# Optimization experiments

Measured on AMD Instinct MI355X. Metric: run time of the kernel, lower is better.

Reference implementation:

```python
import jax, jax.numpy as jnp
import numpy as np

# dims matching input_specs / init_kwargs
S_BATCH, T_BATCH, NUM, DIM, H, W = 4, 4, 8, 512, 32, 32
K = 64              # self.k, number of kmeans clusters
KMEANS_ITERS = 10   # fixed Lloyd iterations (stand-in for kmeans-to-convergence)


def _kmeans(points):
    """Euclidean Lloyd kmeans. points: [n, d] -> centers [K, d].
    Deterministic init: first K points. Empty clusters keep old center."""
    centers0 = points[:K]
    sq_p = jnp.sum(points * points, axis=1)  # [n]

    def step(centers, _):
        # squared euclidean distance [n, K]
        d2 = sq_p[:, None] + jnp.sum(centers * centers, axis=1)[None, :] \
             - 2.0 * points @ centers.T
        assign = jnp.argmin(d2, axis=1)                      # [n]
        onehot = jax.nn.one_hot(assign, K, dtype=points.dtype)  # [n, K]
        counts = onehot.sum(axis=0)                          # [K]
        sums = onehot.T @ points                             # [K, d]
        new = jnp.where(counts[:, None] > 0,
                        sums / jnp.maximum(counts, 1.0)[:, None],
                        centers)
        return new, None

    centers, _ = jax.lax.scan(step, centers0, None, length=KMEANS_ITERS)
    return centers


def setup_inputs() -> dict:
    key = jax.random.key(0)
    k1, k2, k3, k4 = jax.random.split(key, 4)
    return {
        "source_feat": jax.random.normal(k1, (S_BATCH, NUM, DIM, H, W), dtype=jnp.float32),
        "target_feat": jax.random.normal(k2, (T_BATCH, NUM, DIM, H, W), dtype=jnp.float32),
        "source_label": jax.random.randint(k3, (S_BATCH,), 0, 10),
        "target_label": jax.random.randint(k4, (T_BATCH,), 0, 10),
    }


def reference(source_feat, target_feat, source_label, target_label):
    sb, num, dim, h, w = source_feat.shape
    tb = target_feat.shape[0]

    # view each map as (h*w, dim) point cloud, kmeans per (batch, num)
    s_pts = source_feat.reshape(sb, num, dim, h * w).transpose(0, 1, 3, 2)
    t_pts = target_feat.reshape(tb, num, dim, h * w).transpose(0, 1, 3, 2)
    km = jax.vmap(jax.vmap(_kmeans))
    cs = km(s_pts).transpose(1, 0, 2, 3)  # [num, sb, K, dim]
    ct = km(t_pts).transpose(1, 0, 2, 3)  # [num, tb, K, dim]

    # mat_dist for every (num, i, j) pair of center sets: [num, sb, tb, K, K]
    sq_s = jnp.sum(cs * cs, axis=-1)  # [num, sb, K]
    sq_t = jnp.sum(ct * ct, axis=-1)  # [num, tb, K]
    dots = jnp.einsum('nikd,njld->nijkl', cs, ct)
    dist = jnp.sqrt(jnp.maximum(
        sq_s[:, :, None, :, None] + sq_t[:, None, :, None, :] - 2.0 * dots, 0.0))
    y = jnp.argmin(dist, axis=-1)  # [num, sb, tb, K] nearest target center per source center

    # gather matched target centers; replicate source centers over j (torch append order: i, j, k)
    ct_b = jnp.broadcast_to(ct[:, None], (num, sb, tb, K, dim))
    t_mat = jnp.take_along_axis(ct_b, y[..., None], axis=3)            # [num, sb, tb, K, dim]
    s_mat = jnp.broadcast_to(cs[:, :, None], (num, sb, tb, K, dim))

    N = sb * tb * K
    s_mat = s_mat.reshape(num, N, dim)
    t_mat = t_mat.reshape(num, N, dim)

    # trans_mat[k] = s_mat.T @ pinv(t_mat.T)   -> [num, dim, dim]
    pinv_t = jnp.linalg.pinv(t_mat.transpose(0, 2, 1))  # pinv([dim, N]) -> [num, N, dim]
    trans_mat = jnp.einsum('nkd,nke->nde', s_mat, pinv_t)
    return trans_mat
```

## Files before the change

kernel.cpp:

```cpp
#include <hip/hip_runtime.h>

typedef unsigned int u32;
typedef unsigned long long u64;

#define NPTS  1024
#define DIMD  512
#define KCL   64
#define KMIT  10

constexpr size_t O_CTG  = 0;
constexpr size_t O_SUMS = O_CTG  + 64ull*512*64;
constexpr size_t O_CNT  = O_SUMS + 64ull*64*512;
constexpr size_t O_SQC  = O_CNT  + 64ull*64;
constexpr size_t O_SQP  = O_SQC  + 64ull*64;
constexpr size_t O_ASG  = O_SQP  + 64ull*1024;
constexpr size_t O_CTN  = O_ASG  + 64ull*1024;
constexpr size_t O_Y    = O_CTN  + 8ull*256*512;
constexpr size_t O_CNT2 = O_Y    + 8ull*4*4*64;
constexpr size_t O_BM   = O_CNT2 + 8ull*256;
constexpr size_t O_G    = O_BM   + 8ull*256*512;
constexpr size_t O_LT   = O_G    + 8ull*256*256;
constexpr size_t O_YB   = O_LT   + 8ull*256*256;
constexpr size_t O_ZB   = O_YB   + 8ull*256*512;
constexpr size_t O_PTST = O_ZB   + 8ull*256*512;

constexpr size_t O_PS0 = O_SUMS;
constexpr size_t O_PS1 = O_CTN;
static_assert(O_PS1 + 64ull*64*512 <= O_G, "PS1 overlay must fit before O_G");

constexpr size_t O_CS = O_SUMS;
constexpr size_t O_W  = O_YB;
constexpr size_t O_WT = O_YB + 8ull*4*64*64;

__device__ __forceinline__ const float* run_base(const float* s, const float* t, int run){
    const float* b = (run < 32) ? s : t;
    return b + (size_t)(run & 31) * (DIMD * NPTS);
}
__device__ __forceinline__ u64 dpack(float d2, int c){
    u32 u = __float_as_uint(d2);
    u = (u & 0x80000000u) ? ~u : (u | 0x80000000u);
    return ((u64)u << 32) | (u32)c;
}
__device__ __forceinline__ float rdlane(float v, int l){
    return __uint_as_float(__builtin_amdgcn_readlane(__float_as_uint(v), l));
}

__global__ __launch_bounds__(256) void k_init(const float* __restrict__ src, const float* __restrict__ tgt,
                                              float* __restrict__ ws){
    int bx = blockIdx.x; int run = bx >> 2, q = bx & 3;
    int tid = threadIdx.x;
    const float* base = run_base(src, tgt, run);
    int p = q*256 + tid;
    float acc = 0.f;
    for (int d = 0; d < DIMD; ++d){
        float v = base[(size_t)d*NPTS + p];
        acc = fmaf(v, v, acc);
    }
    ws[O_SQP + run*NPTS + p] = acc;
    if (q == 0){
        if (tid < KCL) ws[O_SQC + run*KCL + tid] = acc;
        if (tid < KCL) ((int*)(ws + O_CNT))[run*KCL + tid] = 0;
        for (int idx = tid; idx < DIMD*KCL; idx += 256){
            int d = idx >> 6, c = idx & 63;
            ws[O_CTG + (size_t)run*DIMD*KCL + idx] = base[(size_t)d*NPTS + c];
        }
    }
}

__global__ __launch_bounds__(256) void k_ptsT(const float* __restrict__ src, const float* __restrict__ tgt,
                                              float* __restrict__ ws){
    int bx = blockIdx.x; int dt = bx & 7, pt = (bx >> 3) & 15, run = bx >> 7;
    int tid = threadIdx.x, lane = tid & 63, r4 = tid >> 6;
    const float* base = run_base(src, tgt, run);
    __shared__ float t[64*65];
    for (int pass = 0; pass < 16; ++pass){
        int r = pass*4 + r4;
        t[r*65 + lane] = base[(size_t)(dt*64 + r)*NPTS + pt*64 + lane];
    }
    __syncthreads();
    for (int pass = 0; pass < 16; ++pass){
        int p = pass*4 + r4;
        ws[O_PTST + ((size_t)run*NPTS + pt*64 + p)*DIMD + dt*64 + lane] = t[lane*65 + p];
    }
}

__global__ __launch_bounds__(256) void k_assign(const float* __restrict__ src, const float* __restrict__ tgt,
                                                const float* __restrict__ ctr, const float* __restrict__ sqc,
                                                const float* __restrict__ sqp,
                                                int* __restrict__ asg, int* __restrict__ cnt){
    int bx = blockIdx.x; int run = bx >> 3, qt = bx & 7;
    int tid = threadIdx.x, lane = tid & 63;
    int g = __builtin_amdgcn_readfirstlane(tid >> 6);
    const float* base = run_base(src, tgt, run);
    const float* cg = ctr + (size_t)run*DIMD*KCL + g*16;
    int p0 = qt*128 + 2*lane;
    float acc[2][16] = {};
    __shared__ u64 red[4][128];

#define LOADP(P, DB) { \
    _Pragma("unroll") \
    for (int u = 0; u < 8; ++u) \
        P[u] = *(const float2*)&base[(size_t)((DB)*8 + u)*NPTS + p0]; }

#define COMPUTE(P, DB) { \
    _Pragma("unroll") \
    for (int u = 0; u < 8; ++u){ \
        const float4* cp = (const float4*)(cg + (size_t)((DB)*8 + u)*KCL); \
        float4 c0 = cp[0], c1 = cp[1], c2 = cp[2], c3 = cp[3]; \
        float cv[16] = {c0.x,c0.y,c0.z,c0.w, c1.x,c1.y,c1.z,c1.w, \
                        c2.x,c2.y,c2.z,c2.w, c3.x,c3.y,c3.z,c3.w}; \
        _Pragma("unroll") \
        for (int cl = 0; cl < 16; ++cl){ \
            acc[0][cl] = fmaf(P[u].x, cv[cl], acc[0][cl]); \
            acc[1][cl] = fmaf(P[u].y, cv[cl], acc[1][cl]); \
        } \
    } }

    float2 pa[8], pb[8];
    LOADP(pa, 0);
    for (int db = 0; db < 64; db += 2){
        if (db + 1 < 64) LOADP(pb, db + 1);
        COMPUTE(pa, db);
        if (db + 2 < 64) LOADP(pa, db + 2);
        COMPUTE(pb, db + 1);
    }
#undef LOADP
#undef COMPUTE

    const float* sqcg = sqc + run*KCL + g*16;
    float sq[16];
    #pragma unroll
    for (int q = 0; q < 16; ++q) sq[q] = sqcg[q];
    float2 sq2 = *(const float2*)&sqp[run*NPTS + p0];
    #pragma unroll
    for (int s = 0; s < 2; ++s){
        float sqpv = s ? sq2.y : sq2.x;
        u64 best = dpack(sqpv + sq[0] - 2.f*acc[s][0], g*16);
        #pragma unroll
        for (int cl = 1; cl < 16; ++cl){
            u64 k2 = dpack(sqpv + sq[cl] - 2.f*acc[s][cl], g*16 + cl);
            best = (k2 < best) ? k2 : best;
        }
        red[g][2*lane + s] = best;
    }
    __syncthreads();
    if (tid < 128){
        u64 b = red[0][tid];
        #pragma unroll
        for (int g2 = 1; g2 < 4; ++g2){ u64 k2 = red[g2][tid]; b = (k2 < b) ? k2 : b; }
        int c = (int)(b & 0xffffffffu);
        asg[run*NPTS + qt*128 + tid] = c;
        atomicAdd(&cnt[run*KCL + c], 1);
    }
}

__global__ __launch_bounds__(256) void k_sums(float* __restrict__ ws){
    int bx = blockIdx.x; int pg = bx & 1, dh = (bx >> 1) & 1, run = bx >> 2;
    int tid = threadIdx.x;
    __shared__ float sm[KCL*256];
    __shared__ int a[512];
    const int* asg = (const int*)(ws + O_ASG);
    for (int idx = tid; idx < 512; idx += 256) a[idx] = asg[run*NPTS + pg*512 + idx];
    for (int idx = tid; idx < KCL*256; idx += 256) sm[idx] = 0.f;
    __syncthreads();
    const float* pT = ws + O_PTST + ((size_t)run*NPTS + pg*512)*DIMD + dh*256 + tid;
    for (int p = 0; p < 512; p += 4){
        float v0 = pT[(size_t)(p+0)*DIMD], v1 = pT[(size_t)(p+1)*DIMD];
        float v2 = pT[(size_t)(p+2)*DIMD], v3 = pT[(size_t)(p+3)*DIMD];
        sm[a[p+0]*256 + tid] += v0;
        sm[a[p+1]*256 + tid] += v1;
        sm[a[p+2]*256 + tid] += v2;
        sm[a[p+3]*256 + tid] += v3;
    }
    __syncthreads();
    size_t psx = pg ? O_PS1 : O_PS0;
    for (int c = 0; c < KCL; ++c)
        ws[psx + ((size_t)run*KCL + c)*DIMD + dh*256 + tid] = sm[c*256 + tid];
}

__global__ __launch_bounds__(256) void k_newc(float* __restrict__ ws){
    int run = blockIdx.x, tid = threadIdx.x;
    __shared__ float sm2[KCL*65];
    __shared__ int cl[KCL];
    int* cnt = (int*)(ws + O_CNT);
    if (tid < KCL) cl[tid] = cnt[run*KCL + tid];
    __syncthreads();
    if (tid < KCL) cnt[run*KCL + tid] = 0;
    float sqa = 0.f;
    for (int dc = 0; dc < 8; ++dc){
        for (int idx = tid; idx < KCL*64; idx += 256){
            int c = idx >> 6, dl = idx & 63;
            size_t o = ((size_t)run*KCL + c)*DIMD + dc*64 + dl;
            sm2[c*65 + dl] = ws[O_PS0 + o] + ws[O_PS1 + o];
        }
        __syncthreads();
        for (int idx = tid; idx < KCL*64; idx += 256){
            int dl = idx >> 6, c = idx & 63, d = dc*64 + dl;
            size_t gi = O_CTG + (size_t)run*DIMD*KCL + d*KCL + c;
            float old = ws[gi];
            int cc = cl[c];
            float nv = (cc > 0) ? sm2[c*65 + dl] / (float)cc : old;
            ws[gi] = nv;
            sm2[c*65 + dl] = nv;
        }
        __syncthreads();
        if (tid < KCL){
            for (int dl = 0; dl < 64; ++dl){ float v = sm2[tid*65 + dl]; sqa = fmaf(v, v, sqa); }
        }
        __syncthreads();
    }
    if (tid < KCL) ws[O_SQC + run*KCL + tid] = sqa;
}

__global__ __launch_bounds__(256) void k_ctn(float* __restrict__ ws){
    int bx = blockIdx.x; int dc = bx & 7, jj = (bx >> 3) & 3, n = (bx >> 5) & 7, st = bx >> 8;
    int run = st ? (jj*8 + n) : (32 + jj*8 + n);
    int tid = threadIdx.x, lane = tid & 63, r4 = tid >> 6;
    __shared__ float t[64*65];
    for (int pass = 0; pass < 16; ++pass){
        int r = pass*4 + r4;
        t[r*65 + lane] = ws[O_CTG + (size_t)run*DIMD*KCL + (dc*64 + r)*KCL + lane];
    }
    __syncthreads();
    size_t dstbase = st ? (O_CS  + ((size_t)(n*4 + jj)*64)*DIMD)
                        : (O_CTN + ((size_t)n*256 + jj*64)*DIMD);
    for (int pass = 0; pass < 16; ++pass){
        int l = pass*4 + r4;
        ws[dstbase + (size_t)l*DIMD + dc*64 + lane] = t[lane*65 + l];
    }
}

__global__ __launch_bounds__(256) void k_map(float* __restrict__ ws){
    int bx = blockIdx.x; int j = bx & 3, i = (bx >> 2) & 3, n = bx >> 4;
    int run_s = i*8 + n, run_t = 32 + j*8 + n;
    int tid = threadIdx.x, lane = tid & 63;
    int g = __builtin_amdgcn_readfirstlane(tid >> 6);
    const float* cgs = ws + O_CTG + (size_t)run_s*DIMD*KCL + lane;
    const float* cgt = ws + O_CTG + (size_t)run_t*DIMD*KCL + g*16;
    float acc[16] = {};
    for (int d = 0; d < DIMD; ++d){
        float csv = cgs[d*KCL];
        const float4* cp = (const float4*)(cgt + d*KCL);
        float4 c0=cp[0], c1=cp[1], c2=cp[2], c3=cp[3];
        float cv[16] = {c0.x,c0.y,c0.z,c0.w, c1.x,c1.y,c1.z,c1.w,
                        c2.x,c2.y,c2.z,c2.w, c3.x,c3.y,c3.z,c3.w};
        #pragma unroll
        for (int cl = 0; cl < 16; ++cl) acc[cl] = fmaf(csv, cv[cl], acc[cl]);
    }
    float sqs = ws[O_SQC + run_s*KCL + lane];
    const float* sqtp = ws + O_SQC + run_t*KCL + g*16;
    u64 best = dpack(sqs + sqtp[0] - 2.f*acc[0], g*16);
    #pragma unroll
    for (int cl = 1; cl < 16; ++cl){
        u64 k2 = dpack(sqs + sqtp[cl] - 2.f*acc[cl], g*16 + cl);
        best = (k2 < best) ? k2 : best;
    }
    __shared__ u64 red[4][64];
    red[g][lane] = best;
    __syncthreads();
    if (tid < 64){
        u64 b = red[0][tid];
        #pragma unroll
        for (int g2 = 1; g2 < 4; ++g2){ u64 k2 = red[g2][tid]; b = (k2 < b) ? k2 : b; }
        int l = (int)(b & 0xffffffffu);
        int* yv   = (int*)(ws + O_Y);
        int* cnt2 = (int*)(ws + O_CNT2);
        yv[((n*4 + i)*4 + j)*64 + tid] = l;
        atomicAdd(&cnt2[n*256 + j*64 + l], 1);
    }
}

__global__ __launch_bounds__(256) void k_bmat(float* __restrict__ ws){
    int bx = blockIdx.x; int dh = bx & 1, j = (bx >> 1) & 3, n = bx >> 3;
    int tid = threadIdx.x;
    __shared__ float Bacc[KCL*256];
    __shared__ int yl[256];
    __shared__ int c2[KCL];
    const int* yv   = (const int*)(ws + O_Y);
    const int* cnt2 = (const int*)(ws + O_CNT2);
    { int i = tid >> 6, k = tid & 63; yl[tid] = yv[((n*4 + i)*4 + j)*64 + k]; }
    if (tid < KCL) c2[tid] = cnt2[n*256 + j*64 + tid];
    for (int idx = tid; idx < KCL*256; idx += 256) Bacc[idx] = 0.f;
    __syncthreads();
    const float* cs = ws + O_CS + (size_t)(n*4)*64*DIMD + dh*256 + tid;
    #pragma unroll 4
    for (int s = 0; s < 256; ++s){
        int l = yl[s];
        float v = cs[(size_t)s*DIMD];
        Bacc[l*256 + tid] += v;
    }
    __syncthreads();
    for (int l = 0; l < KCL; ++l){
        int cc = c2[l]; if (cc < 1) cc = 1;
        ws[O_BM + ((size_t)n*256 + j*64 + l)*DIMD + dh*256 + tid] = Bacc[l*256 + tid] / (float)cc;
    }
}

__global__ __launch_bounds__(256) void k_gram(float* __restrict__ ws){
    int bx = blockIdx.x; int cc = bx & 7, n = bx >> 3;
    int tid = threadIdx.x, llane = tid & 63, jlane = tid >> 6;
    int run_t = 32 + jlane*8 + n;
    const float* bbase = ws + O_CTG + (size_t)run_t*DIMD*KCL + llane;
    const float* arow  = ws + O_CTN + (size_t)(n*256 + cc*32)*DIMD;
    float acc[32] = {};
    for (int d = 0; d < DIMD; d += 4){
        float bv0 = bbase[(d+0)*KCL], bv1 = bbase[(d+1)*KCL];
        float bv2 = bbase[(d+2)*KCL], bv3 = bbase[(d+3)*KCL];
        #pragma unroll
        for (int c = 0; c < 32; ++c){
            const float4 av = *(const float4*)&arow[c*DIMD + d];
            acc[c] = fmaf(av.x, bv0, acc[c]);
            acc[c] = fmaf(av.y, bv1, acc[c]);
            acc[c] = fmaf(av.z, bv2, acc[c]);
            acc[c] = fmaf(av.w, bv3, acc[c]);
        }
    }
    const int* cnt2 = (const int*)(ws + O_CNT2);
    bool used_cp = cnt2[n*256 + tid] > 0;
    float* Gp = ws + O_G + (size_t)n*65536;
    #pragma unroll
    for (int c = 0; c < 32; ++c){
        int cg = cc*32 + c;
        bool used_c = cnt2[n*256 + cg] > 0;
        float v = (used_c && used_cp) ? acc[c] : ((cg == tid) ? 1.f : 0.f);
        Gp[(size_t)cg*256 + tid] = v;
    }
}

__global__ __launch_bounds__(256, 1) void k_chol(float* __restrict__ ws){
    int n = blockIdx.x, tid = threadIdx.x;
    int lane = tid & 63, wv = tid >> 6;
    float* Gn  = ws + O_G  + (size_t)n*65536;
    float* LTn = ws + O_LT + (size_t)n*65536;
    __shared__ __align__(16) float Pc[64*200];

    for (int kb = 0; kb < 4; ++kb){
        int c0 = kb*64, r1 = c0 + 64, rem = 256 - r1;
        float dreg[64];
        {
            const float* grow = Gn + (size_t)(c0+lane)*256 + c0;
            #pragma unroll
            for (int j4 = 0; j4 < 16; ++j4){
                float4 v = *(const float4*)&grow[j4*4];
                dreg[j4*4+0]=v.x; dreg[j4*4+1]=v.y; dreg[j4*4+2]=v.z; dreg[j4*4+3]=v.w;
            }
        }
        float preg[64];
        int prow = (wv-1)*64 + lane;
        bool pact = (wv >= 1) && (prow < rem);
        {
            const float* growp = Gn + (size_t)(r1+prow)*256 + c0;
            #pragma unroll
            for (int j4 = 0; j4 < 16; ++j4){
                if (pact){
                    float4 v = *(const float4*)&growp[j4*4];
                    preg[j4*4+0]=v.x; preg[j4*4+1]=v.y; preg[j4*4+2]=v.z; preg[j4*4+3]=v.w;
                } else {
                    preg[j4*4+0]=0.f; preg[j4*4+1]=0.f; preg[j4*4+2]=0.f; preg[j4*4+3]=0.f;
                }
            }
        }
        #pragma unroll
        for (int k = 0; k < 64; ++k){
            float dkk = sqrtf(fmaxf(rdlane(dreg[k], k), 1e-30f));
            float inv = 1.f / dkk;
            dreg[k] = (lane == k) ? dkk : dreg[k]*inv;
            preg[k] *= inv;
            #pragma unroll
            for (int j = k+1; j < 64; ++j){
                float s = rdlane(dreg[k], j);
                dreg[j] = fmaf(-dreg[k], s, dreg[j]);
                preg[j] = fmaf(-preg[k], s, preg[j]);
            }
        }
        if (wv == 0){
            float* grow = Gn + (size_t)(c0+lane)*256 + c0;
            #pragma unroll
            for (int j4 = 0; j4 < 16; ++j4){
                float4 v; v.x=dreg[j4*4+0]; v.y=dreg[j4*4+1]; v.z=dreg[j4*4+2]; v.w=dreg[j4*4+3];
                *(float4*)&grow[j4*4] = v;
            }
        }
        if (pact){
            float* growp = Gn + (size_t)(r1+prow)*256 + c0;
            #pragma unroll
            for (int j4 = 0; j4 < 16; ++j4){
                float4 v; v.x=preg[j4*4+0]; v.y=preg[j4*4+1]; v.z=preg[j4*4+2]; v.w=preg[j4*4+3];
                *(float4*)&growp[j4*4] = v;
            }
            float* ltp = LTn + (size_t)c0*256 + r1 + prow;
            #pragma unroll
            for (int j = 0; j < 64; ++j) ltp[(size_t)j*256] = preg[j];
            #pragma unroll
            for (int j = 0; j < 64; ++j) Pc[j*200 + prow] = preg[j];
        }
        __syncthreads();
        if (rem > 0){
            int nt4 = rem >> 2;
            int ntiles = nt4*(nt4+1)/2;
            for (int t = tid; t < ntiles; t += 256){
                int ti = (int)((sqrtf(8.f*(float)t + 1.f) - 1.f) * 0.5f);
                while ((ti+1)*(ti+2)/2 <= t) ++ti;
                while (ti*(ti+1)/2 > t) --ti;
                int tj = t - ti*(ti+1)/2;
                int i0 = ti*4, j0 = tj*4;
                float acc[4][4] = {};
                for (int k = 0; k < 64; ++k){
                    const float4 pi = *(const float4*)&Pc[k*200 + i0];
                    const float4 pj = *(const float4*)&Pc[k*200 + j0];
                    float pir[4] = {pi.x,pi.y,pi.z,pi.w};
                    float pjr[4] = {pj.x,pj.y,pj.z,pj.w};
                    #pragma unroll
                    for (int r = 0; r < 4; ++r)
                        #pragma unroll
                        for (int s = 0; s < 4; ++s)
                            acc[r][s] = fmaf(pir[r], pjr[s], acc[r][s]);
                }
                #pragma unroll
                for (int r = 0; r < 4; ++r){
                    float* grow = Gn + (size_t)(r1+i0+r)*256 + r1 + j0;
                    #pragma unroll
                    for (int s = 0; s < 4; ++s) grow[s] -= acc[r][s];
                }
            }
        }
        __syncthreads();
    }
}

__global__ __launch_bounds__(256, 1) void k_dinv(float* __restrict__ ws){
    int n = blockIdx.x, tid = threadIdx.x;
    int lane = tid & 63, kb = tid >> 6;
    const float* Gn = ws + O_G + (size_t)n*65536;
    __shared__ __align__(16) float DlT[4][64*65];
    for (int idx = lane; idx < 1024; idx += 64){
        int r = idx >> 4, c4 = idx & 15;
        float4 v = *(const float4*)&Gn[(size_t)(kb*64 + r)*256 + kb*64 + c4*4];
        DlT[kb][(c4*4+0)*65 + r] = v.x;
        DlT[kb][(c4*4+1)*65 + r] = v.y;
        DlT[kb][(c4*4+2)*65 + r] = v.z;
        DlT[kb][(c4*4+3)*65 + r] = v.w;
    }
    __syncthreads();
    float x[64];
    #pragma unroll
    for (int i = 0; i < 64; ++i) x[i] = (i == lane) ? 1.f : 0.f;
    const float* Dk = DlT[kb];
    #pragma unroll
    for (int k = 0; k < 64; ++k){
        float invd = 1.f / Dk[k*65 + k];
        x[k] *= invd;
        #pragma unroll
        for (int i = k+1; i < 64; ++i)
            x[i] = fmaf(-Dk[k*65 + i], x[k], x[i]);
    }
    float* Wg  = ws + O_W  + ((size_t)n*4 + kb)*4096;
    float* WTg = ws + O_WT + ((size_t)n*4 + kb)*4096;
    #pragma unroll
    for (int r = 0; r < 64; ++r) Wg[r*64 + lane] = x[r];
    #pragma unroll
    for (int r4 = 0; r4 < 16; ++r4){
        float4 v; v.x=x[r4*4+0]; v.y=x[r4*4+1]; v.z=x[r4*4+2]; v.w=x[r4*4+3];
        *(float4*)&WTg[lane*64 + r4*4] = v;
    }
}

__global__ __launch_bounds__(256, 1) void k_solve(float* __restrict__ ws){
    int n = blockIdx.x, cg = blockIdx.y;
    int tid = threadIdx.x;
    int tx = tid & 15, ty = tid >> 4;
    const float* Gn  = ws + O_G  + (size_t)n*65536;
    const float* LTn = ws + O_LT + (size_t)n*65536;
    const float* Ct  = ws + O_CTN + (size_t)n*256*DIMD + (size_t)cg*64;
    const float* Wg  = ws + O_W  + (size_t)n*4*4096;
    const float* WTg = ws + O_WT + (size_t)n*4*4096;
    float* Zb = ws + O_ZB + (size_t)n*256*DIMD + (size_t)cg*64;

    __shared__ __align__(16) float YL[4][64*65];
    __shared__ __align__(16) float At[64*65];
    __shared__ __align__(16) float RL[64*65];

    float acc[4][4];
    for (int bi = 0; bi < 4; ++bi){
        #pragma unroll
        for (int a = 0; a < 4; ++a){
            float4 v = *(const float4*)&Ct[(size_t)(bi*64 + ty*4 + a)*DIMD + tx*4];
            acc[a][0]=v.x; acc[a][1]=v.y; acc[a][2]=v.z; acc[a][3]=v.w;
        }
        for (int j = 0; j < bi; ++j){
            __syncthreads();
            for (int idx = tid; idx < 1024; idx += 256){
                int k = idx >> 4, r4 = idx & 15;
                float4 v = *(const float4*)&LTn[(size_t)(j*64 + k)*256 + bi*64 + r4*4];
                *(float4*)&At[k*65 + r4*4] = v;
            }
            __syncthreads();
            const float* Yj = YL[j];
            #pragma unroll 8
            for (int k = 0; k < 64; ++k){
                float4 av = *(const float4*)&At[k*65 + ty*4];
                float4 yv = *(const float4*)&Yj[k*65 + tx*4];
                float ar[4] = {av.x,av.y,av.z,av.w};
                float yr[4] = {yv.x,yv.y,yv.z,yv.w};
                #pragma unroll
                for (int a = 0; a < 4; ++a)
                    #pragma unroll
                    for (int b = 0; b < 4; ++b)
                        acc[a][b] = fmaf(-ar[a], yr[b], acc[a][b]);
            }
        }
        __syncthreads();
        #pragma unroll
        for (int a = 0; a < 4; ++a){
            float4 v; v.x=acc[a][0]; v.y=acc[a][1]; v.z=acc[a][2]; v.w=acc[a][3];
            *(float4*)&RL[(ty*4 + a)*65 + tx*4] = v;
        }
        for (int idx = tid; idx < 1024; idx += 256){
            int k = idx >> 4, r4 = idx & 15;
            float4 v = *(const float4*)&WTg[(size_t)bi*4096 + k*64 + r4*4];
            *(float4*)&At[k*65 + r4*4] = v;
        }
        __syncthreads();
        float out[4][4] = {};
        #pragma unroll 8
        for (int k = 0; k < 64; ++k){
            float4 av = *(const float4*)&At[k*65 + ty*4];
            float4 rv = *(const float4*)&RL[k*65 + tx*4];
            float ar[4] = {av.x,av.y,av.z,av.w};
            float rr[4] = {rv.x,rv.y,rv.z,rv.w};
            #pragma unroll
            for (int a = 0; a < 4; ++a)
                #pragma unroll
                for (int b = 0; b < 4; ++b)
                    out[a][b] = fmaf(ar[a], rr[b], out[a][b]);
        }
        float* Yi = YL[bi];
        #pragma unroll
        for (int a = 0; a < 4; ++a){
            float4 v; v.x=out[a][0]; v.y=out[a][1]; v.z=out[a][2]; v.w=out[a][3];
            *(float4*)&Yi[(ty*4 + a)*65 + tx*4] = v;
        }
    }
    for (int bi = 3; bi >= 0; --bi){
        __syncthreads();
        #pragma unroll
        for (int a = 0; a < 4; ++a){
            float4 v = *(const float4*)&YL[bi][(ty*4 + a)*65 + tx*4];
            acc[a][0]=v.x; acc[a][1]=v.y; acc[a][2]=v.z; acc[a][3]=v.w;
        }
        for (int j = bi+1; j < 4; ++j){
            __syncthreads();
            for (int idx = tid; idx < 1024; idx += 256){
                int k = idx >> 4, r4 = idx & 15;
                float4 v = *(const float4*)&Gn[(size_t)(j*64 + k)*256 + bi*64 + r4*4];
                *(float4*)&At[k*65 + r4*4] = v;
            }
            __syncthreads();
            const float* Zj = YL[j];
            #pragma unroll 8
            for (int k = 0; k < 64; ++k){
                float4 av = *(const float4*)&At[k*65 + ty*4];
                float4 zv = *(const float4*)&Zj[k*65 + tx*4];
                float ar[4] = {av.x,av.y,av.z,av.w};
                float zr[4] = {zv.x,zv.y,zv.z,zv.w};
                #pragma unroll
                for (int a = 0; a < 4; ++a)
                    #pragma unroll
                    for (int b = 0; b < 4; ++b)
                        acc[a][b] = fmaf(-ar[a], zr[b], acc[a][b]);
            }
        }
        __syncthreads();
        #pragma unroll
        for (int a = 0; a < 4; ++a){
            float4 v; v.x=acc[a][0]; v.y=acc[a][1]; v.z=acc[a][2]; v.w=acc[a][3];
            *(float4*)&RL[(ty*4 + a)*65 + tx*4] = v;
        }
        for (int idx = tid; idx < 1024; idx += 256){
            int k = idx >> 4, r4 = idx & 15;
            float4 v = *(const float4*)&Wg[(size_t)bi*4096 + k*64 + r4*4];
            *(float4*)&At[k*65 + r4*4] = v;
        }
        __syncthreads();
        float out[4][4] = {};
        #pragma unroll 8
        for (int k = 0; k < 64; ++k){
            float4 av = *(const float4*)&At[k*65 + ty*4];
            float4 rv = *(const float4*)&RL[k*65 + tx*4];
            float ar[4] = {av.x,av.y,av.z,av.w};
            float rr[4] = {rv.x,rv.y,rv.z,rv.w};
            #pragma unroll
            for (int a = 0; a < 4; ++a)
                #pragma unroll
                for (int b = 0; b < 4; ++b)
                    out[a][b] = fmaf(ar[a], rr[b], out[a][b]);
        }
        float* Zi = YL[bi];
        #pragma unroll
        for (int a = 0; a < 4; ++a){
            float4 v; v.x=out[a][0]; v.y=out[a][1]; v.z=out[a][2]; v.w=out[a][3];
            *(float4*)&Zi[(ty*4 + a)*65 + tx*4] = v;
            *(float4*)&Zb[(size_t)(bi*64 + ty*4 + a)*DIMD + tx*4] = v;
        }
    }
}

__global__ __launch_bounds__(256) void k_gemmE(const float* __restrict__ ws, float* __restrict__ out){
    int bx = blockIdx.x; int et = bx & 7, dt = (bx >> 3) & 7, n = bx >> 6;
    int tid = threadIdx.x;
    __shared__ float Bl[256*64];
    __shared__ float Zl[256*64];
    const float* Bm = ws + O_BM + (size_t)n*256*DIMD;
    const float* Zb = ws + O_ZB + (size_t)n*256*DIMD;
    for (int idx = tid; idx < 16384; idx += 256){
        int c = idx >> 6, dd = idx & 63;
        Bl[idx] = Bm[(size_t)c*DIMD + dt*64 + dd];
        Zl[idx] = Zb[(size_t)c*DIMD + et*64 + dd];
    }
    __syncthreads();
    int td = tid & 15, te = tid >> 4;
    float acc[4][4] = {};
    for (int c = 0; c < 256; ++c){
        float4 bv = *(const float4*)&Bl[c*64 + td*4];
        float4 zv = *(const float4*)&Zl[c*64 + te*4];
        float b4[4] = {bv.x, bv.y, bv.z, bv.w};
        float z4[4] = {zv.x, zv.y, zv.z, zv.w};
        #pragma unroll
        for (int r = 0; r < 4; ++r)
            #pragma unroll
            for (int s = 0; s < 4; ++s) acc[r][s] = fmaf(b4[r], z4[s], acc[r][s]);
    }
    float* ob = out + (size_t)n*262144 + (size_t)(dt*64 + td*4)*DIMD + et*64 + te*4;
    #pragma unroll
    for (int r = 0; r < 4; ++r){
        float4 o; o.x = acc[r][0]; o.y = acc[r][1]; o.z = acc[r][2]; o.w = acc[r][3];
        *(float4*)&ob[(size_t)r*DIMD] = o;
    }
}

extern "C" void kernel_launch(void* const* d_in, const int* in_sizes, int n_in,
                              void* d_out, int out_size, void* d_ws, size_t ws_size,
                              hipStream_t stream){
    const float* src = (const float*)d_in[0];
    const float* tgt = (const float*)d_in[1];
    float* ws  = (float*)d_ws;
    float* out = (float*)d_out;

    k_init<<<256, 256, 0, stream>>>(src, tgt, ws);
    k_ptsT<<<8192, 256, 0, stream>>>(src, tgt, ws);

    for (int it = 0; it < KMIT; ++it){
        k_assign<<<512, 256, 0, stream>>>(src, tgt,
                                          ws + O_CTG, ws + O_SQC, ws + O_SQP,
                                          (int*)(ws + O_ASG), (int*)(ws + O_CNT));
        k_sums<<<256, 256, 0, stream>>>(ws);
        k_newc<<<64, 256, 0, stream>>>(ws);
    }

    hipMemsetAsync((char*)d_ws + O_CNT2*4, 0, 8*256*4, stream);
    k_ctn<<<512, 256, 0, stream>>>(ws);
    k_map<<<128, 256, 0, stream>>>(ws);
    k_bmat<<<64, 256, 0, stream>>>(ws);
    k_gram<<<64, 256, 0, stream>>>(ws);
    k_chol<<<8, 256, 0, stream>>>(ws);
    k_dinv<<<8, 256, 0, stream>>>(ws);
    k_solve<<<dim3(8, 8), 256, 0, stream>>>(ws);
    k_gemmE<<<512, 256, 0, stream>>>(ws, out);
}
```

Baseline: 2.635 ms.

## Split kmeans assign over cluster halves and add separate argmin-merge kernel

The assignment kernel now splits the 64 clusters into two halves across blocks, doubling the grid to 1024 blocks. Each wave handles 8 clusters instead of 16, which halves the accumulator registers, and launch bounds request 4 blocks per CU for more occupancy. Each block writes packed (distance, index) candidates to a workspace buffer, and a new k_amin kernel takes the min of the two halves, writes the assignment and does the count atomics. The cost is an extra launch per iteration, and every point column is now loaded twice, once per cluster half.

```diff
diff --git a/kernel.cpp b/kernel.cpp
--- a/kernel.cpp
+++ b/kernel.cpp
@@ -28,6 +28,8 @@
 constexpr size_t O_PS1 = O_CTN;
 static_assert(O_PS1 + 64ull*64*512 <= O_G, "PS1 overlay must fit before O_G");
 
+constexpr size_t O_BEST = O_G;
+
 constexpr size_t O_CS = O_SUMS;
 constexpr size_t O_W  = O_YB;
 constexpr size_t O_WT = O_YB + 8ull*4*64*64;
@@ -84,17 +86,21 @@
     }
 }
 
-__global__ __launch_bounds__(256) void k_assign(const float* __restrict__ src, const float* __restrict__ tgt,
-                                                const float* __restrict__ ctr, const float* __restrict__ sqc,
-                                                const float* __restrict__ sqp,
-                                                int* __restrict__ asg, int* __restrict__ cnt){
-    int bx = blockIdx.x; int run = bx >> 3, qt = bx & 7;
+__global__ __launch_bounds__(256, 4) void k_assign(const float* __restrict__ src, const float* __restrict__ tgt,
+                                                   const float* __restrict__ ctr, const float* __restrict__ sqc,
+                                                   const float* __restrict__ sqp,
+                                                   u64* __restrict__ bestg){
+    int bxx = blockIdx.x;
+    int cb  = (bxx >> 3) & 1;
+    int w   = ((bxx >> 4) << 3) | (bxx & 7);
+    int run = w >> 3, qt = w & 7;
     int tid = threadIdx.x, lane = tid & 63;
     int g = __builtin_amdgcn_readfirstlane(tid >> 6);
+    int c0 = cb*32 + g*8;
     const float* base = run_base(src, tgt, run);
-    const float* cg = ctr + (size_t)run*DIMD*KCL + g*16;
+    const float* cg = ctr + (size_t)run*DIMD*KCL + c0;
     int p0 = qt*128 + 2*lane;
-    float acc[2][16] = {};
+    float acc[2][8] = {};
     __shared__ u64 red[4][128];
 
 #define LOADP(P, DB) { \
@@ -106,11 +112,10 @@
     _Pragma("unroll") \
     for (int u = 0; u < 8; ++u){ \
         const float4* cp = (const float4*)(cg + (size_t)((DB)*8 + u)*KCL); \
-        float4 c0 = cp[0], c1 = cp[1], c2 = cp[2], c3 = cp[3]; \
-        float cv[16] = {c0.x,c0.y,c0.z,c0.w, c1.x,c1.y,c1.z,c1.w, \
-                        c2.x,c2.y,c2.z,c2.w, c3.x,c3.y,c3.z,c3.w}; \
+        float4 c0v = cp[0], c1v = cp[1]; \
+        float cv[8] = {c0v.x,c0v.y,c0v.z,c0v.w, c1v.x,c1v.y,c1v.z,c1v.w}; \
         _Pragma("unroll") \
-        for (int cl = 0; cl < 16; ++cl){ \
+        for (int cl = 0; cl < 8; ++cl){ \
             acc[0][cl] = fmaf(P[u].x, cv[cl], acc[0][cl]); \
             acc[1][cl] = fmaf(P[u].y, cv[cl], acc[1][cl]); \
         } \
@@ -127,18 +132,18 @@
 #undef LOADP
 #undef COMPUTE
 
-    const float* sqcg = sqc + run*KCL + g*16;
-    float sq[16];
-    #pragma unroll
-    for (int q = 0; q < 16; ++q) sq[q] = sqcg[q];
+    const float* sqcg = sqc + run*KCL + c0;
+    float sq[8];
+    #pragma unroll
+    for (int q = 0; q < 8; ++q) sq[q] = sqcg[q];
     float2 sq2 = *(const float2*)&sqp[run*NPTS + p0];
     #pragma unroll
     for (int s = 0; s < 2; ++s){
         float sqpv = s ? sq2.y : sq2.x;
-        u64 best = dpack(sqpv + sq[0] - 2.f*acc[s][0], g*16);
-        #pragma unroll
-        for (int cl = 1; cl < 16; ++cl){
-            u64 k2 = dpack(sqpv + sq[cl] - 2.f*acc[s][cl], g*16 + cl);
+        u64 best = dpack(sqpv + sq[0] - 2.f*acc[s][0], c0);
+        #pragma unroll
+        for (int cl = 1; cl < 8; ++cl){
+            u64 k2 = dpack(sqpv + sq[cl] - 2.f*acc[s][cl], c0 + cl);
             best = (k2 < best) ? k2 : best;
         }
         red[g][2*lane + s] = best;
@@ -148,10 +153,22 @@
         u64 b = red[0][tid];
         #pragma unroll
         for (int g2 = 1; g2 < 4; ++g2){ u64 k2 = red[g2][tid]; b = (k2 < b) ? k2 : b; }
-        int c = (int)(b & 0xffffffffu);
-        asg[run*NPTS + qt*128 + tid] = c;
-        atomicAdd(&cnt[run*KCL + c], 1);
-    }
+        bestg[(((size_t)(run*8 + qt)*128 + tid) << 1) + cb] = b;
+    }
+}
+
+__global__ __launch_bounds__(256) void k_amin(const u64* __restrict__ bestg,
+                                              int* __restrict__ asg, int* __restrict__ cnt){
+    int bx = blockIdx.x; int run = bx >> 2, q = bx & 3;
+    int tid = threadIdx.x;
+    int p = q*256 + tid;
+    int qt = p >> 7, t = p & 127;
+    const u64* bp = bestg + (((size_t)(run*8 + qt)*128 + t) << 1);
+    u64 a = bp[0], b = bp[1];
+    u64 m = (b < a) ? b : a;
+    int c = (int)(m & 0xffffffffu);
+    asg[run*NPTS + p] = c;
+    atomicAdd(&cnt[run*KCL + c], 1);
 }
 
 __global__ __launch_bounds__(256) void k_sums(float* __restrict__ ws){
@@ -650,9 +667,11 @@
     k_ptsT<<<8192, 256, 0, stream>>>(src, tgt, ws);
 
     for (int it = 0; it < KMIT; ++it){
-        k_assign<<<512, 256, 0, stream>>>(src, tgt,
-                                          ws + O_CTG, ws + O_SQC, ws + O_SQP,
-                                          (int*)(ws + O_ASG), (int*)(ws + O_CNT));
+        k_assign<<<1024, 256, 0, stream>>>(src, tgt,
+                                           ws + O_CTG, ws + O_SQC, ws + O_SQP,
+                                           (u64*)(ws + O_BEST));
+        k_amin<<<256, 256, 0, stream>>>((const u64*)(ws + O_BEST),
+                                        (int*)(ws + O_ASG), (int*)(ws + O_CNT));
         k_sums<<<256, 256, 0, stream>>>(ws);
         k_newc<<<64, 256, 0, stream>>>(ws);
     }
```

New measurement: 2.455 ms. 1.07x faster.
